# Performance work log

Hardware: AMD Instinct MI355X
Metric: run time of the kernel (lower is better)

The kernel has to match this reference:

```python
import jax, jax.numpy as jnp
import numpy as np

N_NODES = 100000
N_EDGES = 1600000
N_GRAPHS = 64
IN_CH, HID_CH, OUT_CH, N_CLS = 128, 128, 64, 2


def setup_inputs() -> dict:
    key = jax.random.key(0)
    ks = jax.random.split(key, 8)
    x = jax.random.normal(ks[0], (N_NODES, IN_CH), dtype=jnp.float32)
    edge_index = jax.random.randint(ks[1], (2, N_EDGES), 0, N_NODES)
    batch = jnp.sort(jax.random.randint(ks[2], (N_NODES,), 0, N_GRAPHS))
    glorot = lambda k, shp: jax.random.normal(k, shp, dtype=jnp.float32) / np.float32(np.sqrt(shp[0]))
    return {
        "x": x, "edge_index": edge_index, "batch": batch,
        "W1": glorot(ks[3], (IN_CH, HID_CH)), "b1": jnp.zeros((HID_CH,), jnp.float32),
        "W2": glorot(ks[4], (HID_CH, HID_CH)), "b2": jnp.zeros((HID_CH,), jnp.float32),
        "W3": glorot(ks[5], (HID_CH, OUT_CH)), "b3": jnp.zeros((OUT_CH,), jnp.float32),
        "Wfc": glorot(ks[6], (OUT_CH, N_CLS)), "bfc": jnp.zeros((N_CLS,), jnp.float32),
    }


def gcn_conv(x, src, dst, W, b):
    """PyG GCNConv: add self-loops, D^{-1/2} (A+I) D^{-1/2} (x W) + b."""
    n = x.shape[0]
    h = x @ W  # [N, out]
    # degree with self-loops: 1 + in-degree at dst
    deg = jnp.ones((n,), h.dtype).at[dst].add(1.0)
    dinv = jax.lax.rsqrt(deg)  # deg >= 1 always (self-loop)
    norm = dinv[src] * dinv[dst]  # [E]
    agg = jnp.zeros_like(h).at[dst].add(h[src] * norm[:, None])
    agg = agg + h * (dinv * dinv)[:, None]  # self-loop messages
    return agg + b


def global_mean_pool(x, batch, num_graphs):
    s = jax.ops.segment_sum(x, batch, num_segments=num_graphs)
    cnt = jax.ops.segment_sum(jnp.ones((x.shape[0],), x.dtype), batch, num_segments=num_graphs)
    return s / jnp.maximum(cnt, 1.0)[:, None]


def reference(x, edge_index, batch, W1, b1, W2, b2, W3, b3, Wfc, bfc):
    src, dst = edge_index[0], edge_index[1]
    h = jax.nn.relu(gcn_conv(x, src, dst, W1, b1))   # dropout p=0.0 (eval) -> identity
    h = jax.nn.relu(gcn_conv(h, src, dst, W2, b2))
    h = gcn_conv(h, src, dst, W3, b3)
    g = global_mean_pool(h, batch, N_GRAPHS)          # [G, OUT_CH]
    return g @ Wfc + bfc                              # [G, N_CLS]
```

## Files before the change

kernel.cpp:

```cpp
#include <hip/hip_runtime.h>
#include <hip/hip_bf16.h>


#define THREADS 256
#define BSHIFT 9
#define BSIZE 512

typedef __attribute__((ext_vector_type(8))) short short8;
typedef __attribute__((ext_vector_type(16))) float floatx16;

__device__ __forceinline__ unsigned f2bf(float f) {
    unsigned u = __float_as_uint(f);
    return (u + 0x7fffu + ((u >> 16) & 1u)) >> 16;
}

__device__ __forceinline__ void bf8_acc(uint4 v, float* ac) {
    ac[0] += __uint_as_float(v.x << 16);
    ac[1] += __uint_as_float(v.x & 0xffff0000u);
    ac[2] += __uint_as_float(v.y << 16);
    ac[3] += __uint_as_float(v.y & 0xffff0000u);
    ac[4] += __uint_as_float(v.z << 16);
    ac[5] += __uint_as_float(v.z & 0xffff0000u);
    ac[6] += __uint_as_float(v.w << 16);
    ac[7] += __uint_as_float(v.w & 0xffff0000u);
}


__global__ __launch_bounds__(THREADS) void bucket_count(const int* __restrict__ dst,
                                                        int* __restrict__ btotal,
                                                        int E, int nbuck) {
    __shared__ int cnt[BSIZE];
    for (int i = threadIdx.x; i < nbuck; i += THREADS) cnt[i] = 0;
    __syncthreads();
    for (int e = blockIdx.x * THREADS + threadIdx.x; e < E; e += gridDim.x * THREADS)
        atomicAdd(&cnt[dst[e] >> BSHIFT], 1);
    __syncthreads();
    for (int i = threadIdx.x; i < nbuck; i += THREADS) {
        int c = cnt[i];
        if (c) atomicAdd(&btotal[i], c);
    }
}

__global__ __launch_bounds__(512) void bucket_scan(const int* __restrict__ btotal,
                                                   int* __restrict__ bbase,
                                                   int* __restrict__ bcursor,
                                                   float* __restrict__ gsum,
                                                   int nbuck, int E) {
    __shared__ int lds[512];
    int t = threadIdx.x;
    for (int i = t; i < 64 * 64; i += 512) gsum[i] = 0.0f;
    int v = (t < nbuck) ? btotal[t] : 0;
    lds[t] = v;
    __syncthreads();
    for (int off = 1; off < 512; off <<= 1) {
        int tv = (t >= off) ? lds[t - off] : 0;
        __syncthreads();
        lds[t] += tv;
        __syncthreads();
    }
    if (t < nbuck) {
        int excl = lds[t] - v;
        bbase[t] = excl;
        bcursor[t] = excl;
    }
    if (t == 0) bbase[nbuck] = E;
}

__global__ __launch_bounds__(THREADS) void bucket_scatter(const int* __restrict__ src,
                                                          const int* __restrict__ dst,
                                                          int* __restrict__ bcursor,
                                                          int* __restrict__ pairs, int E) {
    __shared__ int cnt[BSIZE];
    __shared__ int base[BSIZE];
    for (int i = threadIdx.x; i < BSIZE; i += THREADS) cnt[i] = 0;
    __syncthreads();
    int e0 = blockIdx.x * 2048;
    int myb[8], myrank[8], mypk[8];
#pragma unroll
    for (int j = 0; j < 8; ++j) {
        int e = e0 + j * THREADS + threadIdx.x;
        myb[j] = -1;
        if (e < E) {
            int d = dst[e];
            mypk[j] = (src[e] << BSHIFT) | (d & (BSIZE - 1));
            myb[j] = d >> BSHIFT;
            myrank[j] = atomicAdd(&cnt[myb[j]], 1);
        }
    }
    __syncthreads();
    for (int i = threadIdx.x; i < BSIZE; i += THREADS) {
        int c = cnt[i];
        base[i] = c ? atomicAdd(&bcursor[i], c) : 0;
    }
    __syncthreads();
#pragma unroll
    for (int j = 0; j < 8; ++j)
        if (myb[j] >= 0) pairs[(size_t)base[myb[j]] + myrank[j]] = mypk[j];
}

__global__ __launch_bounds__(512) void bucket_fill(const int* __restrict__ pairs,
                                                   const int* __restrict__ bbase,
                                                   int* __restrict__ row_start,
                                                   float* __restrict__ dinv,
                                                   int* __restrict__ esrc,
                                                   int N, int E, int nbuck) {
    __shared__ int cnt[BSIZE];
    __shared__ int scn[BSIZE];
    int b = blockIdx.x, t = threadIdx.x;
    int s = bbase[b], e = bbase[b + 1];
    cnt[t] = 0;
    __syncthreads();
    for (int i = s + t; i < e; i += 512) atomicAdd(&cnt[pairs[i] & (BSIZE - 1)], 1);
    __syncthreads();
    int v = cnt[t];
    scn[t] = v;
    __syncthreads();
    for (int off = 1; off < 512; off <<= 1) {
        int tv = (t >= off) ? scn[t - off] : 0;
        __syncthreads();
        scn[t] += tv;
        __syncthreads();
    }
    int excl = scn[t] - v;
    int g = (b << BSHIFT) + t;
    if (g < N) {
        row_start[g] = s + excl;
        dinv[g] = rsqrtf(1.0f + (float)v);
    }
    if (b == nbuck - 1 && t == 0) row_start[N] = E;
    scn[t] = excl;
    __syncthreads();
    for (int i = s + t; i < e; i += 512) {
        int p = pairs[i];
        int r = atomicAdd(&scn[p & (BSIZE - 1)], 1);
        esrc[s + r] = ((unsigned)p) >> BSHIFT;
    }
}

__device__ __forceinline__ void wt_pack(const float* W, uint4* Wtp, int C, int li) {
    int c = li >> 4, ch = li & 15;
    unsigned r[8];
#pragma unroll
    for (int j = 0; j < 8; ++j) r[j] = f2bf(W[(size_t)(ch * 8 + j) * C + c]);
    uint4 o;
    o.x = r[0] | (r[1] << 16);
    o.y = r[2] | (r[3] << 16);
    o.z = r[4] | (r[5] << 16);
    o.w = r[6] | (r[7] << 16);
    Wtp[li] = o;
}

__global__ __launch_bounds__(THREADS) void prep_wt_all(const float* __restrict__ W1,
                                                       const float* __restrict__ W2,
                                                       const float* __restrict__ W3,
                                                       uint4* __restrict__ Wt1,
                                                       uint4* __restrict__ Wt2,
                                                       uint4* __restrict__ Wt3) {
    int idx = blockIdx.x * THREADS + threadIdx.x;
    if (idx < 2048) wt_pack(W1, Wt1, 128, idx);
    else if (idx < 4096) wt_pack(W2, Wt2, 128, idx - 2048);
    else if (idx < 5120) wt_pack(W3, Wt3, 64, idx - 4096);
}

__global__ __launch_bounds__(THREADS) void prep_x(const float* __restrict__ x,
                                                  const float* __restrict__ dinv,
                                                  uint4* __restrict__ Z, int n) {
    int idx = blockIdx.x * THREADS + threadIdx.x;
    if (idx >= n * 16) return;
    int r = idx >> 4, c = idx & 15;
    float dv = dinv[r];
    const float* p = x + (size_t)r * 128 + c * 8;
    float4 a = *(const float4*)p;
    float4 b = *(const float4*)(p + 4);
    uint4 o;
    o.x = f2bf(a.x * dv) | (f2bf(a.y * dv) << 16);
    o.y = f2bf(a.z * dv) | (f2bf(a.w * dv) << 16);
    o.z = f2bf(b.x * dv) | (f2bf(b.y * dv) << 16);
    o.w = f2bf(b.z * dv) | (f2bf(b.w * dv) << 16);
    Z[idx] = o;
}

__global__ __launch_bounds__(THREADS) void fused_layer(const uint4* __restrict__ Z,
                                                       const uint4* __restrict__ Wt,
                                                       const int* __restrict__ row_start,
                                                       const int* __restrict__ esrc,
                                                       const float* __restrict__ dinv,
                                                       const float* __restrict__ bias,
                                                       uint4* __restrict__ out, int n) {
    __shared__ __align__(16) uint4 ldsX[64 * 16];
    int row0 = blockIdx.x * 64;
    int maxr = n - row0;
    if (maxr > 64) maxr = 64;
    int tid = threadIdx.x;
    int lane = tid & 15, grp = tid >> 4;

    for (int round = 0; round < 4; ++round) {
        int r = round * 16 + grp;
        int node = row0 + r;
        int nd = (node < n) ? node : (n - 1);
        float ac[8] = {0, 0, 0, 0, 0, 0, 0, 0};
        bf8_acc(Z[(size_t)nd * 16 + lane], ac);
        int s = row_start[nd], e = row_start[nd + 1];
        int i = s;
        for (; i + 8 <= e; i += 8) {
            int s0 = esrc[i], s1 = esrc[i + 1], s2 = esrc[i + 2], s3 = esrc[i + 3];
            int s4 = esrc[i + 4], s5 = esrc[i + 5], s6 = esrc[i + 6], s7 = esrc[i + 7];
            uint4 v0 = Z[(size_t)s0 * 16 + lane];
            uint4 v1 = Z[(size_t)s1 * 16 + lane];
            uint4 v2 = Z[(size_t)s2 * 16 + lane];
            uint4 v3 = Z[(size_t)s3 * 16 + lane];
            uint4 v4 = Z[(size_t)s4 * 16 + lane];
            uint4 v5 = Z[(size_t)s5 * 16 + lane];
            uint4 v6 = Z[(size_t)s6 * 16 + lane];
            uint4 v7 = Z[(size_t)s7 * 16 + lane];
            bf8_acc(v0, ac); bf8_acc(v1, ac); bf8_acc(v2, ac); bf8_acc(v3, ac);
            bf8_acc(v4, ac); bf8_acc(v5, ac); bf8_acc(v6, ac); bf8_acc(v7, ac);
        }
        for (; i + 4 <= e; i += 4) {
            int s0 = esrc[i], s1 = esrc[i + 1], s2 = esrc[i + 2], s3 = esrc[i + 3];
            uint4 v0 = Z[(size_t)s0 * 16 + lane];
            uint4 v1 = Z[(size_t)s1 * 16 + lane];
            uint4 v2 = Z[(size_t)s2 * 16 + lane];
            uint4 v3 = Z[(size_t)s3 * 16 + lane];
            bf8_acc(v0, ac); bf8_acc(v1, ac); bf8_acc(v2, ac); bf8_acc(v3, ac);
        }
        for (; i < e; ++i) bf8_acc(Z[(size_t)esrc[i] * 16 + lane], ac);
        float dv = dinv[nd];
        uint4 o;
        o.x = f2bf(ac[0] * dv) | (f2bf(ac[1] * dv) << 16);
        o.y = f2bf(ac[2] * dv) | (f2bf(ac[3] * dv) << 16);
        o.z = f2bf(ac[4] * dv) | (f2bf(ac[5] * dv) << 16);
        o.w = f2bf(ac[6] * dv) | (f2bf(ac[7] * dv) << 16);
        ldsX[r * 16 + (lane ^ (r & 7))] = o;
    }
    __syncthreads();

    int l = tid & 63, wv = tid >> 6;
    int l31 = l & 31, half = l >> 5;
    int nt = wv & 1, mt0 = (wv >> 1) * 2;
    floatx16 acc[2];
#pragma unroll
    for (int t = 0; t < 2; ++t)
#pragma unroll
        for (int q = 0; q < 16; ++q) acc[t][q] = 0.0f;
    int xrow = nt * 32 + l31, xsw = xrow & 7;
#pragma unroll
    for (int kt = 0; kt < 8; ++kt) {
        int chunk = kt * 2 + half;
        short8 xf = *(const short8*)&ldsX[xrow * 16 + (chunk ^ xsw)];
#pragma unroll
        for (int t = 0; t < 2; ++t) {
            int c = (mt0 + t) * 32 + l31;
            short8 wf = *(const short8*)&Wt[c * 16 + chunk];
            acc[t] = __builtin_amdgcn_mfma_f32_32x32x16_bf16(wf, xf, acc[t], 0, 0, 0);
        }
    }
    __syncthreads();

    int node = nt * 32 + l31;
    float dv = (node < maxr) ? dinv[row0 + node] : 0.0f;
    char* outb = (char*)ldsX;
#pragma unroll
    for (int t = 0; t < 2; ++t) {
        int cb = (mt0 + t) * 32;
#pragma unroll
        for (int q = 0; q < 4; ++q) {
            float v[4];
#pragma unroll
            for (int m = 0; m < 4; ++m) {
                int ch = cb + 8 * q + 4 * half + m;
                float x_ = acc[t][q * 4 + m] + bias[ch];
                x_ = fmaxf(x_, 0.0f);
                v[m] = x_ * dv;
            }
            uint2 pk = make_uint2(f2bf(v[0]) | (f2bf(v[1]) << 16),
                                  f2bf(v[2]) | (f2bf(v[3]) << 16));
            int chunk = (cb >> 3) + q;
            *(uint2*)(outb + node * 256 + ((chunk ^ (node & 7)) * 16) + half * 8) = pk;
        }
    }
    __syncthreads();
    for (int idx = tid; idx < maxr * 16; idx += THREADS) {
        int r = idx >> 4, c = idx & 15;
        out[(size_t)(row0 + r) * 16 + c] = *(uint4*)(outb + r * 256 + ((c ^ (r & 7)) * 16));
    }
}

__global__ __launch_bounds__(THREADS) void gemm3(const uint4* __restrict__ Z,
                                                 const uint4* __restrict__ Wt,
                                                 uint4* __restrict__ out, int n) {
    __shared__ __align__(16) uint4 ldsX[64 * 16];
    int row0 = blockIdx.x * 64;
    int maxr = n - row0;
    if (maxr > 64) maxr = 64;
    int tid = threadIdx.x;
    for (int idx = tid; idx < 1024; idx += THREADS) {
        int r = idx >> 4, c = idx & 15;
        uint4 o = (r < maxr) ? Z[(size_t)(row0 + r) * 16 + c] : make_uint4(0, 0, 0, 0);
        ldsX[r * 16 + (c ^ (r & 7))] = o;
    }
    __syncthreads();
    int l = tid & 63, wv = tid >> 6;
    int l31 = l & 31, half = l >> 5;
    int nt = wv & 1, mt = wv >> 1;
    floatx16 acc;
#pragma unroll
    for (int q = 0; q < 16; ++q) acc[q] = 0.0f;
    int xrow = nt * 32 + l31, xsw = xrow & 7;
#pragma unroll
    for (int kt = 0; kt < 8; ++kt) {
        int chunk = kt * 2 + half;
        short8 xf = *(const short8*)&ldsX[xrow * 16 + (chunk ^ xsw)];
        int c = mt * 32 + l31;
        short8 wf = *(const short8*)&Wt[c * 16 + chunk];
        acc = __builtin_amdgcn_mfma_f32_32x32x16_bf16(wf, xf, acc, 0, 0, 0);
    }
    __syncthreads();
    int node = nt * 32 + l31;
    char* outb = (char*)ldsX;
    int cb = mt * 32;
#pragma unroll
    for (int q = 0; q < 4; ++q) {
        uint2 pk = make_uint2(f2bf(acc[q * 4 + 0]) | (f2bf(acc[q * 4 + 1]) << 16),
                              f2bf(acc[q * 4 + 2]) | (f2bf(acc[q * 4 + 3]) << 16));
        int chunk = (cb >> 3) + q;
        *(uint2*)(outb + node * 128 + ((chunk ^ (node & 7)) * 16) + half * 8) = pk;
    }
    __syncthreads();
    for (int idx = tid; idx < maxr * 8; idx += THREADS) {
        int r = idx >> 3, c = idx & 7;
        out[(size_t)(row0 + r) * 8 + c] = *(uint4*)(outb + r * 128 + ((c ^ (r & 7)) * 16));
    }
}

__global__ __launch_bounds__(THREADS) void agg_pool(const uint4* __restrict__ Ps,
                                                    const int* __restrict__ row_start,
                                                    const int* __restrict__ esrc,
                                                    const float* __restrict__ dinv,
                                                    const float* __restrict__ bias,
                                                    const int* __restrict__ batch,
                                                    float* __restrict__ gsum, int n) {
    __shared__ float gpart[32][65];
    __shared__ int used[32];
    int tid = threadIdx.x;
    int lane = tid & 7, grp = tid >> 3;
    int node = blockIdx.x * 32 + grp;
    if (tid < 32) used[tid] = 0;
    for (int idx = tid; idx < 2048; idx += THREADS) gpart[idx >> 6][idx & 63] = 0.0f;
    __syncthreads();
    int gmin = batch[blockIdx.x * 32];
    if (node < n) {
        float ac[8] = {0, 0, 0, 0, 0, 0, 0, 0};
        bf8_acc(Ps[(size_t)node * 8 + lane], ac);
        int s = row_start[node], e = row_start[node + 1];
        int i = s;
        for (; i + 8 <= e; i += 8) {
            int s0 = esrc[i], s1 = esrc[i + 1], s2 = esrc[i + 2], s3 = esrc[i + 3];
            int s4 = esrc[i + 4], s5 = esrc[i + 5], s6 = esrc[i + 6], s7 = esrc[i + 7];
            uint4 v0 = Ps[(size_t)s0 * 8 + lane];
            uint4 v1 = Ps[(size_t)s1 * 8 + lane];
            uint4 v2 = Ps[(size_t)s2 * 8 + lane];
            uint4 v3 = Ps[(size_t)s3 * 8 + lane];
            uint4 v4 = Ps[(size_t)s4 * 8 + lane];
            uint4 v5 = Ps[(size_t)s5 * 8 + lane];
            uint4 v6 = Ps[(size_t)s6 * 8 + lane];
            uint4 v7 = Ps[(size_t)s7 * 8 + lane];
            bf8_acc(v0, ac); bf8_acc(v1, ac); bf8_acc(v2, ac); bf8_acc(v3, ac);
            bf8_acc(v4, ac); bf8_acc(v5, ac); bf8_acc(v6, ac); bf8_acc(v7, ac);
        }
        for (; i + 4 <= e; i += 4) {
            int s0 = esrc[i], s1 = esrc[i + 1], s2 = esrc[i + 2], s3 = esrc[i + 3];
            uint4 v0 = Ps[(size_t)s0 * 8 + lane];
            uint4 v1 = Ps[(size_t)s1 * 8 + lane];
            uint4 v2 = Ps[(size_t)s2 * 8 + lane];
            uint4 v3 = Ps[(size_t)s3 * 8 + lane];
            bf8_acc(v0, ac); bf8_acc(v1, ac); bf8_acc(v2, ac); bf8_acc(v3, ac);
        }
        for (; i < e; ++i) bf8_acc(Ps[(size_t)esrc[i] * 8 + lane], ac);
        float dv = dinv[node];
        float4 b0 = ((const float4*)bias)[lane * 2];
        float4 b1 = ((const float4*)bias)[lane * 2 + 1];
        float h[8];
        h[0] = fmaf(dv, ac[0], b0.x); h[1] = fmaf(dv, ac[1], b0.y);
        h[2] = fmaf(dv, ac[2], b0.z); h[3] = fmaf(dv, ac[3], b0.w);
        h[4] = fmaf(dv, ac[4], b1.x); h[5] = fmaf(dv, ac[5], b1.y);
        h[6] = fmaf(dv, ac[6], b1.z); h[7] = fmaf(dv, ac[7], b1.w);
        int g = batch[node];
        int slot = g - gmin;
        if (slot < 32) {
            if (lane == 0) used[slot] = 1;
#pragma unroll
            for (int j = 0; j < 8; ++j) atomicAdd(&gpart[slot][lane * 8 + j], h[j]);
        } else {
#pragma unroll
            for (int j = 0; j < 8; ++j) atomicAdd(&gsum[(size_t)g * 64 + lane * 8 + j], h[j]);
        }
    }
    __syncthreads();
    for (int idx = tid; idx < 2048; idx += THREADS) {
        int s = idx >> 6, ch = idx & 63;
        if (used[s]) atomicAdd(&gsum[(size_t)(gmin + s) * 64 + ch], gpart[s][ch]);
    }
}

__device__ __forceinline__ int dev_lower_bound(const int* a, int n, int key) {
    int lo = 0, hi = n;
    while (lo < hi) {
        int mid = (lo + hi) >> 1;
        if (a[mid] < key) lo = mid + 1;
        else hi = mid;
    }
    return lo;
}

__global__ __launch_bounds__(128) void finalize_fc(const float* __restrict__ gsum,
                                                   const int* __restrict__ batch, int n,
                                                   const float* __restrict__ Wfc,
                                                   const float* __restrict__ bfc,
                                                   float* __restrict__ out) {
    __shared__ float gm[64 * 64];
    __shared__ float cnt[64];
    int t = threadIdx.x;
    if (t < 64)
        cnt[t] = (float)(dev_lower_bound(batch, n, t + 1) - dev_lower_bound(batch, n, t));
    __syncthreads();
    for (int i = t; i < 64 * 64; i += 128) gm[i] = gsum[i] / fmaxf(cnt[i >> 6], 1.0f);
    __syncthreads();
    int g = t >> 1, cls = t & 1;
    float acc = bfc[cls];
    for (int c = 0; c < 64; ++c) acc = fmaf(gm[g * 64 + c], Wfc[c * 2 + cls], acc);
    out[g * 2 + cls] = acc;
}

extern "C" void kernel_launch(void* const* d_in, const int* in_sizes, int n_in,
                              void* d_out, int out_size, void* d_ws, size_t ws_size,
                              hipStream_t stream) {
    const float* x    = (const float*)d_in[0];
    const int*   ei   = (const int*)d_in[1];
    const int*   batch= (const int*)d_in[2];
    const float* W1   = (const float*)d_in[3];
    const float* b1   = (const float*)d_in[4];
    const float* W2   = (const float*)d_in[5];
    const float* b2   = (const float*)d_in[6];
    const float* W3   = (const float*)d_in[7];
    const float* b3   = (const float*)d_in[8];
    const float* Wfc  = (const float*)d_in[9];
    const float* bfc  = (const float*)d_in[10];
    float* out = (float*)d_out;

    const int N = in_sizes[2];
    const int E = in_sizes[1] / 2;
    const int* esrc_in = ei;
    const int* edst_in = ei + E;
    const int nbuck = (N + BSIZE - 1) >> BSHIFT;

    uint4* bufA      = (uint4*)d_ws;
    uint4* bufB      = bufA + (size_t)N * 16;
    uint4* bufC      = bufB + (size_t)N * 16;
    int*   pairs     = (int*)(bufC + (size_t)N * 8);
    int*   esrc      = pairs + E;
    int*   row_start = esrc + E;
    float* dinv      = (float*)(row_start + N + 1);
    int*   btotal    = (int*)(dinv + N);
    int*   bbase     = btotal + 512;
    int*   bcursor   = bbase + 513;
    float* gsum      = (float*)(bcursor + 512);
    uint4* Wt1       = (uint4*)(gsum + 64 * 64);
    uint4* Wt2       = Wt1 + 2048;
    uint4* Wt3       = Wt2 + 2048;

    hipMemsetAsync(btotal, 0, 512 * sizeof(int), stream);
    bucket_count<<<512, THREADS, 0, stream>>>(edst_in, btotal, E, nbuck);
    bucket_scan<<<1, 512, 0, stream>>>(btotal, bbase, bcursor, gsum, nbuck, E);
    bucket_scatter<<<(E + 2047) / 2048, THREADS, 0, stream>>>(esrc_in, edst_in, bcursor, pairs, E);
    bucket_fill<<<nbuck, 512, 0, stream>>>(pairs, bbase, row_start, dinv, esrc, N, E, nbuck);
    prep_wt_all<<<20, THREADS, 0, stream>>>(W1, W2, W3, Wt1, Wt2, Wt3);
    prep_x<<<(N * 16 + THREADS - 1) / THREADS, THREADS, 0, stream>>>(x, dinv, bufA, N);

    const int GB = (N + 63) / 64;

    fused_layer<<<GB, THREADS, 0, stream>>>(bufA, Wt1, row_start, esrc, dinv, b1, bufB, N);
    fused_layer<<<GB, THREADS, 0, stream>>>(bufB, Wt2, row_start, esrc, dinv, b2, bufA, N);
    gemm3<<<GB, THREADS, 0, stream>>>(bufA, Wt3, bufC, N);
    agg_pool<<<(N + 31) / 32, THREADS, 0, stream>>>(bufC, row_start, esrc, dinv, b3, batch, gsum, N);

    finalize_fc<<<1, 128, 0, stream>>>(gsum, batch, N, Wfc, bfc, out);
}
```

Before: 433.4 us.

## Store layer-3 features as fp8, fold prep kernels into bucket stages, move bias to finalize

Layer-3 GEMM output is now encoded to fp8 e4m3 (software encode and decode) instead of bf16, halving the bytes gathered per edge in the final aggregation. The weight packing is folded into the scan kernel and the x scaling/bf16 conversion into bucket_fill, removing two launches and a dinv reread. The bucket count now writes per-block partial histograms instead of using global atomics, which removes the memset. Bias b3 is added after mean pooling instead of per node. fp8 precision loss and the ALU-heavy decode are the risks.

```diff
diff --git a/kernel.cpp b/kernel.cpp
--- a/kernel.cpp
+++ b/kernel.cpp
@@ -5,6 +5,7 @@
 #define THREADS 256
 #define BSHIFT 9
 #define BSIZE 512
+#define CNTB 128
 
 typedef __attribute__((ext_vector_type(8))) short short8;
 typedef __attribute__((ext_vector_type(16))) float floatx16;
@@ -25,31 +26,88 @@
     ac[7] += __uint_as_float(v.w & 0xffff0000u);
 }
 
+__device__ __forceinline__ float fp8_dec(unsigned b) {
+    unsigned e = (b >> 3) & 15u, m = b & 7u;
+    float vn = __uint_as_float(((e + 120u) << 23) | (m << 20));
+    float vd = (float)m * 0.001953125f;
+    float v = e ? vn : vd;
+    return (b & 0x80u) ? -v : v;
+}
+
+__device__ __forceinline__ unsigned fp8_enc(float f) {
+    unsigned u = __float_as_uint(f);
+    unsigned s = (u >> 31) << 7;
+    float a = fabsf(f);
+    if (a >= 448.0f) return s | 0x7e;
+    if (a < 0.0009765625f) return s;
+    unsigned au = u & 0x7fffffffu;
+    if (a >= 0.015625f) {
+        unsigned r = au + 0x7ffffu + ((au >> 20) & 1u);
+        unsigned e2 = (r >> 23) - 120u;
+        if (e2 > 15u) return s | 0x7e;
+        return s | (e2 << 3) | ((r >> 20) & 7u);
+    } else {
+        int m = (int)(a * 512.0f + 0.5f);
+        if (m > 7) return s | (1u << 3);
+        return s | (unsigned)m;
+    }
+}
+
+__device__ __forceinline__ void fp8x8_acc(uint2 v, float* ac) {
+#pragma unroll
+    for (int j = 0; j < 4; ++j) ac[j] += fp8_dec((v.x >> (8 * j)) & 0xffu);
+#pragma unroll
+    for (int j = 0; j < 4; ++j) ac[4 + j] += fp8_dec((v.y >> (8 * j)) & 0xffu);
+}
+
 
 __global__ __launch_bounds__(THREADS) void bucket_count(const int* __restrict__ dst,
-                                                        int* __restrict__ btotal,
-                                                        int E, int nbuck) {
+                                                        int* __restrict__ bhistpart, int E) {
     __shared__ int cnt[BSIZE];
-    for (int i = threadIdx.x; i < nbuck; i += THREADS) cnt[i] = 0;
-    __syncthreads();
-    for (int e = blockIdx.x * THREADS + threadIdx.x; e < E; e += gridDim.x * THREADS)
+    for (int i = threadIdx.x; i < BSIZE; i += THREADS) cnt[i] = 0;
+    __syncthreads();
+    for (int e = blockIdx.x * THREADS + threadIdx.x; e < E; e += CNTB * THREADS)
         atomicAdd(&cnt[dst[e] >> BSHIFT], 1);
     __syncthreads();
-    for (int i = threadIdx.x; i < nbuck; i += THREADS) {
-        int c = cnt[i];
-        if (c) atomicAdd(&btotal[i], c);
-    }
-}
-
-__global__ __launch_bounds__(512) void bucket_scan(const int* __restrict__ btotal,
+    for (int i = threadIdx.x; i < BSIZE; i += THREADS)
+        bhistpart[blockIdx.x * BSIZE + i] = cnt[i];
+}
+
+__device__ __forceinline__ void wt_pack(const float* W, uint4* Wtp, int C, int li) {
+    int c = li >> 4, ch = li & 15;
+    unsigned r[8];
+#pragma unroll
+    for (int j = 0; j < 8; ++j) r[j] = f2bf(W[(size_t)(ch * 8 + j) * C + c]);
+    uint4 o;
+    o.x = r[0] | (r[1] << 16);
+    o.y = r[2] | (r[3] << 16);
+    o.z = r[4] | (r[5] << 16);
+    o.w = r[6] | (r[7] << 16);
+    Wtp[li] = o;
+}
+
+__global__ __launch_bounds__(512) void bucket_scan(const int* __restrict__ bhistpart,
                                                    int* __restrict__ bbase,
                                                    int* __restrict__ bcursor,
                                                    float* __restrict__ gsum,
+                                                   const float* __restrict__ W1,
+                                                   const float* __restrict__ W2,
+                                                   const float* __restrict__ W3,
+                                                   uint4* __restrict__ Wt1,
+                                                   uint4* __restrict__ Wt2,
+                                                   uint4* __restrict__ Wt3,
                                                    int nbuck, int E) {
     __shared__ int lds[512];
     int t = threadIdx.x;
     for (int i = t; i < 64 * 64; i += 512) gsum[i] = 0.0f;
-    int v = (t < nbuck) ? btotal[t] : 0;
+    for (int i = t; i < 5120; i += 512) {
+        if (i < 2048) wt_pack(W1, Wt1, 128, i);
+        else if (i < 4096) wt_pack(W2, Wt2, 128, i - 2048);
+        else wt_pack(W3, Wt3, 64, i - 4096);
+    }
+    int v = 0;
+    if (t < nbuck)
+        for (int bb = 0; bb < CNTB; ++bb) v += bhistpart[bb * BSIZE + t];
     lds[t] = v;
     __syncthreads();
     for (int off = 1; off < 512; off <<= 1) {
@@ -100,12 +158,15 @@
 
 __global__ __launch_bounds__(512) void bucket_fill(const int* __restrict__ pairs,
                                                    const int* __restrict__ bbase,
+                                                   const float* __restrict__ x,
                                                    int* __restrict__ row_start,
                                                    float* __restrict__ dinv,
                                                    int* __restrict__ esrc,
+                                                   uint4* __restrict__ Z,
                                                    int N, int E, int nbuck) {
     __shared__ int cnt[BSIZE];
     __shared__ int scn[BSIZE];
+    __shared__ float dvs[BSIZE];
     int b = blockIdx.x, t = threadIdx.x;
     int s = bbase[b], e = bbase[b + 1];
     cnt[t] = 0;
@@ -123,9 +184,11 @@
     }
     int excl = scn[t] - v;
     int g = (b << BSHIFT) + t;
+    float dv = rsqrtf(1.0f + (float)v);
+    dvs[t] = dv;
     if (g < N) {
         row_start[g] = s + excl;
-        dinv[g] = rsqrtf(1.0f + (float)v);
+        dinv[g] = dv;
     }
     if (b == nbuck - 1 && t == 0) row_start[N] = E;
     scn[t] = excl;
@@ -135,49 +198,23 @@
         int r = atomicAdd(&scn[p & (BSIZE - 1)], 1);
         esrc[s + r] = ((unsigned)p) >> BSHIFT;
     }
-}
-
-__device__ __forceinline__ void wt_pack(const float* W, uint4* Wtp, int C, int li) {
-    int c = li >> 4, ch = li & 15;
-    unsigned r[8];
-#pragma unroll
-    for (int j = 0; j < 8; ++j) r[j] = f2bf(W[(size_t)(ch * 8 + j) * C + c]);
-    uint4 o;
-    o.x = r[0] | (r[1] << 16);
-    o.y = r[2] | (r[3] << 16);
-    o.z = r[4] | (r[5] << 16);
-    o.w = r[6] | (r[7] << 16);
-    Wtp[li] = o;
-}
-
-__global__ __launch_bounds__(THREADS) void prep_wt_all(const float* __restrict__ W1,
-                                                       const float* __restrict__ W2,
-                                                       const float* __restrict__ W3,
-                                                       uint4* __restrict__ Wt1,
-                                                       uint4* __restrict__ Wt2,
-                                                       uint4* __restrict__ Wt3) {
-    int idx = blockIdx.x * THREADS + threadIdx.x;
-    if (idx < 2048) wt_pack(W1, Wt1, 128, idx);
-    else if (idx < 4096) wt_pack(W2, Wt2, 128, idx - 2048);
-    else if (idx < 5120) wt_pack(W3, Wt3, 64, idx - 4096);
-}
-
-__global__ __launch_bounds__(THREADS) void prep_x(const float* __restrict__ x,
-                                                  const float* __restrict__ dinv,
-                                                  uint4* __restrict__ Z, int n) {
-    int idx = blockIdx.x * THREADS + threadIdx.x;
-    if (idx >= n * 16) return;
-    int r = idx >> 4, c = idx & 15;
-    float dv = dinv[r];
-    const float* p = x + (size_t)r * 128 + c * 8;
-    float4 a = *(const float4*)p;
-    float4 b = *(const float4*)(p + 4);
-    uint4 o;
-    o.x = f2bf(a.x * dv) | (f2bf(a.y * dv) << 16);
-    o.y = f2bf(a.z * dv) | (f2bf(a.w * dv) << 16);
-    o.z = f2bf(b.x * dv) | (f2bf(b.y * dv) << 16);
-    o.w = f2bf(b.z * dv) | (f2bf(b.w * dv) << 16);
-    Z[idx] = o;
+    int base = b << BSHIFT;
+    for (int idx = t; idx < BSIZE * 16; idx += 512) {
+        int r = idx >> 4, c = idx & 15;
+        int node = base + r;
+        if (node < N) {
+            float w = dvs[r];
+            const float* p = x + (size_t)node * 128 + c * 8;
+            float4 a = *(const float4*)p;
+            float4 bb = *(const float4*)(p + 4);
+            uint4 o;
+            o.x = f2bf(a.x * w) | (f2bf(a.y * w) << 16);
+            o.y = f2bf(a.z * w) | (f2bf(a.w * w) << 16);
+            o.z = f2bf(bb.x * w) | (f2bf(bb.y * w) << 16);
+            o.w = f2bf(bb.z * w) | (f2bf(bb.w * w) << 16);
+            Z[(size_t)node * 16 + c] = o;
+        }
+    }
 }
 
 __global__ __launch_bounds__(THREADS) void fused_layer(const uint4* __restrict__ Z,
@@ -321,23 +358,21 @@
     int cb = mt * 32;
 #pragma unroll
     for (int q = 0; q < 4; ++q) {
-        uint2 pk = make_uint2(f2bf(acc[q * 4 + 0]) | (f2bf(acc[q * 4 + 1]) << 16),
-                              f2bf(acc[q * 4 + 2]) | (f2bf(acc[q * 4 + 3]) << 16));
-        int chunk = (cb >> 3) + q;
-        *(uint2*)(outb + node * 128 + ((chunk ^ (node & 7)) * 16) + half * 8) = pk;
-    }
-    __syncthreads();
-    for (int idx = tid; idx < maxr * 8; idx += THREADS) {
-        int r = idx >> 3, c = idx & 7;
-        out[(size_t)(row0 + r) * 8 + c] = *(uint4*)(outb + r * 128 + ((c ^ (r & 7)) * 16));
-    }
-}
-
-__global__ __launch_bounds__(THREADS) void agg_pool(const uint4* __restrict__ Ps,
+        unsigned pk = fp8_enc(acc[q * 4 + 0]) | (fp8_enc(acc[q * 4 + 1]) << 8) |
+                      (fp8_enc(acc[q * 4 + 2]) << 16) | (fp8_enc(acc[q * 4 + 3]) << 24);
+        *(unsigned*)(outb + node * 64 + cb + 8 * q + 4 * half) = pk;
+    }
+    __syncthreads();
+    for (int idx = tid; idx < maxr * 4; idx += THREADS) {
+        int r = idx >> 2, c = idx & 3;
+        out[(size_t)(row0 + r) * 4 + c] = *(uint4*)(outb + r * 64 + c * 16);
+    }
+}
+
+__global__ __launch_bounds__(THREADS) void agg_pool(const uint2* __restrict__ Ps,
                                                     const int* __restrict__ row_start,
                                                     const int* __restrict__ esrc,
                                                     const float* __restrict__ dinv,
-                                                    const float* __restrict__ bias,
                                                     const int* __restrict__ batch,
                                                     float* __restrict__ gsum, int n) {
     __shared__ float gpart[32][65];
@@ -351,49 +386,42 @@
     int gmin = batch[blockIdx.x * 32];
     if (node < n) {
         float ac[8] = {0, 0, 0, 0, 0, 0, 0, 0};
-        bf8_acc(Ps[(size_t)node * 8 + lane], ac);
+        fp8x8_acc(Ps[(size_t)node * 8 + lane], ac);
         int s = row_start[node], e = row_start[node + 1];
         int i = s;
         for (; i + 8 <= e; i += 8) {
             int s0 = esrc[i], s1 = esrc[i + 1], s2 = esrc[i + 2], s3 = esrc[i + 3];
             int s4 = esrc[i + 4], s5 = esrc[i + 5], s6 = esrc[i + 6], s7 = esrc[i + 7];
-            uint4 v0 = Ps[(size_t)s0 * 8 + lane];
-            uint4 v1 = Ps[(size_t)s1 * 8 + lane];
-            uint4 v2 = Ps[(size_t)s2 * 8 + lane];
-            uint4 v3 = Ps[(size_t)s3 * 8 + lane];
-            uint4 v4 = Ps[(size_t)s4 * 8 + lane];
-            uint4 v5 = Ps[(size_t)s5 * 8 + lane];
-            uint4 v6 = Ps[(size_t)s6 * 8 + lane];
-            uint4 v7 = Ps[(size_t)s7 * 8 + lane];
-            bf8_acc(v0, ac); bf8_acc(v1, ac); bf8_acc(v2, ac); bf8_acc(v3, ac);
-            bf8_acc(v4, ac); bf8_acc(v5, ac); bf8_acc(v6, ac); bf8_acc(v7, ac);
+            uint2 v0 = Ps[(size_t)s0 * 8 + lane];
+            uint2 v1 = Ps[(size_t)s1 * 8 + lane];
+            uint2 v2 = Ps[(size_t)s2 * 8 + lane];
+            uint2 v3 = Ps[(size_t)s3 * 8 + lane];
+            uint2 v4 = Ps[(size_t)s4 * 8 + lane];
+            uint2 v5 = Ps[(size_t)s5 * 8 + lane];
+            uint2 v6 = Ps[(size_t)s6 * 8 + lane];
+            uint2 v7 = Ps[(size_t)s7 * 8 + lane];
+            fp8x8_acc(v0, ac); fp8x8_acc(v1, ac); fp8x8_acc(v2, ac); fp8x8_acc(v3, ac);
+            fp8x8_acc(v4, ac); fp8x8_acc(v5, ac); fp8x8_acc(v6, ac); fp8x8_acc(v7, ac);
         }
         for (; i + 4 <= e; i += 4) {
             int s0 = esrc[i], s1 = esrc[i + 1], s2 = esrc[i + 2], s3 = esrc[i + 3];
-            uint4 v0 = Ps[(size_t)s0 * 8 + lane];
-            uint4 v1 = Ps[(size_t)s1 * 8 + lane];
-            uint4 v2 = Ps[(size_t)s2 * 8 + lane];
-            uint4 v3 = Ps[(size_t)s3 * 8 + lane];
-            bf8_acc(v0, ac); bf8_acc(v1, ac); bf8_acc(v2, ac); bf8_acc(v3, ac);
-        }
-        for (; i < e; ++i) bf8_acc(Ps[(size_t)esrc[i] * 8 + lane], ac);
+            uint2 v0 = Ps[(size_t)s0 * 8 + lane];
+            uint2 v1 = Ps[(size_t)s1 * 8 + lane];
+            uint2 v2 = Ps[(size_t)s2 * 8 + lane];
+            uint2 v3 = Ps[(size_t)s3 * 8 + lane];
+            fp8x8_acc(v0, ac); fp8x8_acc(v1, ac); fp8x8_acc(v2, ac); fp8x8_acc(v3, ac);
+        }
+        for (; i < e; ++i) fp8x8_acc(Ps[(size_t)esrc[i] * 8 + lane], ac);
         float dv = dinv[node];
-        float4 b0 = ((const float4*)bias)[lane * 2];
-        float4 b1 = ((const float4*)bias)[lane * 2 + 1];
-        float h[8];
-        h[0] = fmaf(dv, ac[0], b0.x); h[1] = fmaf(dv, ac[1], b0.y);
-        h[2] = fmaf(dv, ac[2], b0.z); h[3] = fmaf(dv, ac[3], b0.w);
-        h[4] = fmaf(dv, ac[4], b1.x); h[5] = fmaf(dv, ac[5], b1.y);
-        h[6] = fmaf(dv, ac[6], b1.z); h[7] = fmaf(dv, ac[7], b1.w);
         int g = batch[node];
         int slot = g - gmin;
         if (slot < 32) {
             if (lane == 0) used[slot] = 1;
 #pragma unroll
-            for (int j = 0; j < 8; ++j) atomicAdd(&gpart[slot][lane * 8 + j], h[j]);
+            for (int j = 0; j < 8; ++j) atomicAdd(&gpart[slot][lane * 8 + j], dv * ac[j]);
         } else {
 #pragma unroll
-            for (int j = 0; j < 8; ++j) atomicAdd(&gsum[(size_t)g * 64 + lane * 8 + j], h[j]);
+            for (int j = 0; j < 8; ++j) atomicAdd(&gsum[(size_t)g * 64 + lane * 8 + j], dv * ac[j]);
         }
     }
     __syncthreads();
@@ -415,6 +443,7 @@
 
 __global__ __launch_bounds__(128) void finalize_fc(const float* __restrict__ gsum,
                                                    const int* __restrict__ batch, int n,
+                                                   const float* __restrict__ b3,
                                                    const float* __restrict__ Wfc,
                                                    const float* __restrict__ bfc,
                                                    float* __restrict__ out) {
@@ -424,7 +453,8 @@
     if (t < 64)
         cnt[t] = (float)(dev_lower_bound(batch, n, t + 1) - dev_lower_bound(batch, n, t));
     __syncthreads();
-    for (int i = t; i < 64 * 64; i += 128) gm[i] = gsum[i] / fmaxf(cnt[i >> 6], 1.0f);
+    for (int i = t; i < 64 * 64; i += 128)
+        gm[i] = gsum[i] / fmaxf(cnt[i >> 6], 1.0f) + b3[i & 63];
     __syncthreads();
     int g = t >> 1, cls = t & 1;
     float acc = bfc[cls];
@@ -457,32 +487,30 @@
     uint4* bufA      = (uint4*)d_ws;
     uint4* bufB      = bufA + (size_t)N * 16;
     uint4* bufC      = bufB + (size_t)N * 16;
-    int*   pairs     = (int*)(bufC + (size_t)N * 8);
+    int*   pairs     = (int*)(bufC + (size_t)N * 4);
     int*   esrc      = pairs + E;
     int*   row_start = esrc + E;
-    float* dinv      = (float*)(row_start + N + 1);
-    int*   btotal    = (int*)(dinv + N);
-    int*   bbase     = btotal + 512;
-    int*   bcursor   = bbase + 513;
+    float* dinv      = (float*)(row_start + N + 4);
+    int*   bhistpart = (int*)(dinv + N);
+    int*   bbase     = bhistpart + CNTB * BSIZE;
+    int*   bcursor   = bbase + 516;
     float* gsum      = (float*)(bcursor + 512);
     uint4* Wt1       = (uint4*)(gsum + 64 * 64);
     uint4* Wt2       = Wt1 + 2048;
     uint4* Wt3       = Wt2 + 2048;
 
-    hipMemsetAsync(btotal, 0, 512 * sizeof(int), stream);
-    bucket_count<<<512, THREADS, 0, stream>>>(edst_in, btotal, E, nbuck);
-    bucket_scan<<<1, 512, 0, stream>>>(btotal, bbase, bcursor, gsum, nbuck, E);
+    bucket_count<<<CNTB, THREADS, 0, stream>>>(edst_in, bhistpart, E);
+    bucket_scan<<<1, 512, 0, stream>>>(bhistpart, bbase, bcursor, gsum,
+                                       W1, W2, W3, Wt1, Wt2, Wt3, nbuck, E);
     bucket_scatter<<<(E + 2047) / 2048, THREADS, 0, stream>>>(esrc_in, edst_in, bcursor, pairs, E);
-    bucket_fill<<<nbuck, 512, 0, stream>>>(pairs, bbase, row_start, dinv, esrc, N, E, nbuck);
-    prep_wt_all<<<20, THREADS, 0, stream>>>(W1, W2, W3, Wt1, Wt2, Wt3);
-    prep_x<<<(N * 16 + THREADS - 1) / THREADS, THREADS, 0, stream>>>(x, dinv, bufA, N);
+    bucket_fill<<<nbuck, 512, 0, stream>>>(pairs, bbase, x, row_start, dinv, esrc, bufA, N, E, nbuck);
 
     const int GB = (N + 63) / 64;
 
     fused_layer<<<GB, THREADS, 0, stream>>>(bufA, Wt1, row_start, esrc, dinv, b1, bufB, N);
     fused_layer<<<GB, THREADS, 0, stream>>>(bufB, Wt2, row_start, esrc, dinv, b2, bufA, N);
     gemm3<<<GB, THREADS, 0, stream>>>(bufA, Wt3, bufC, N);
-    agg_pool<<<(N + 31) / 32, THREADS, 0, stream>>>(bufC, row_start, esrc, dinv, b3, batch, gsum, N);
-
-    finalize_fc<<<1, 128, 0, stream>>>(gsum, batch, N, Wfc, bfc, out);
-}
+    agg_pool<<<(N + 31) / 32, THREADS, 0, stream>>>((const uint2*)bufC, row_start, esrc, dinv, batch, gsum, N);
+
+    finalize_fc<<<1, 128, 0, stream>>>(gsum, batch, N, b3, Wfc, bfc, out);
+}
```

After: 455.4 us. +5.1%, slower.
